# Optimization experiments

Measured on AMD Instinct MI355X. Metric: run time of the kernel, lower is better.

Reference implementation:

```python
import jax, jax.numpy as jnp
import numpy as np

S, H, NH, DS = 4096, 1024, 2, 64   # seq_len, hidden, num_heads, static_in_size
HD = H // NH                        # head_dim = 512
EPS = 1e-5                          # eqx.nn.LayerNorm default eps


def setup_inputs() -> dict:
    key = jax.random.key(0)
    ks = jax.random.split(key, 11)
    sc = lambda n: 1.0 / np.sqrt(n)
    return {
        "inputs": jax.random.normal(ks[0], (S, H), jnp.float32),
        "static_data": jax.random.normal(ks[1], (DS,), jnp.float32),
        "base_mask": jax.random.randint(ks[2], (S,), 0, 2).astype(bool),
        "Wq": jax.random.normal(ks[3], (H, H), jnp.float32) * sc(H),
        "Wk": jax.random.normal(ks[4], (H, H), jnp.float32) * sc(H),
        "Wv": jax.random.normal(ks[5], (H, H), jnp.float32) * sc(H),
        "Wo": jax.random.normal(ks[6], (H, H), jnp.float32) * sc(H),
        "Ws": jax.random.normal(ks[7], (H, DS), jnp.float32) * sc(DS),
        "bs": jax.random.normal(ks[8], (H,), jnp.float32) * 0.01,
        "ln_w": jnp.ones((H,), jnp.float32),
        "ln_b": jnp.zeros((H,), jnp.float32),
    }


def reference(inputs, static_data, base_mask, Wq, Wk, Wv, Wo, Ws, bs, ln_w, ln_b):
    # static embedding injected into keys/values
    semb = Ws @ static_data + bs                      # [H]
    kv_in = inputs + semb[None, :]                    # [S, H]

    # per-head projections (eqx Linear: y = W @ x, no bias in MHA projections)
    q = (inputs @ Wq.T).reshape(S, NH, HD)
    k = (kv_in @ Wk.T).reshape(S, NH, HD)
    v = (kv_in @ Wv.T).reshape(S, NH, HD)

    logits = jnp.einsum('qhd,khd->hqk', q, k) / np.sqrt(HD)  # [NH, S, S]

    # head 0: irregular mask (base_mask broadcast over queries); head 1: all-ones
    irregular = jnp.broadcast_to(base_mask[None, :], (S, S))
    mask = jnp.stack([irregular, jnp.ones((S, S), bool)], axis=0)  # [2, S, S]
    logits = jnp.where(mask, logits, jnp.finfo(logits.dtype).min)

    attn = jax.nn.softmax(logits, axis=-1)
    ctx = jnp.einsum('hqk,khd->qhd', attn, v).reshape(S, H)
    out = ctx @ Wo.T                                  # output projection

    # dropout_rate = 0 -> identity; residual + per-token LayerNorm
    res = out + inputs
    mu = res.mean(-1, keepdims=True)
    var = res.var(-1, keepdims=True)
    return (res - mu) / jnp.sqrt(var + EPS) * ln_w + ln_b
```

## Files before the change

kernel.cpp:

```cpp
#include <hip/hip_runtime.h>
#include <stdint.h>

#define S_LEN  4096
#define HID    1024
#define NHEAD  2
#define HDIM   512
#define NSPLIT 4
#define KS_STRIDE 520
#define LN_EPS 1e-5f

typedef __bf16 bf16x8 __attribute__((ext_vector_type(8)));
typedef float  f32x4  __attribute__((ext_vector_type(4)));

__device__ __forceinline__ float b2f(unsigned short u) {
    return __uint_as_float(((unsigned int)u) << 16);
}
__device__ __forceinline__ unsigned short f2b(float f) {
    unsigned int u = __float_as_uint(f);
    u += 0x7FFFu + ((u >> 16) & 1u);
    return (unsigned short)(u >> 16);
}

__device__ __forceinline__ void async_cp16(const void* g, void* l) {
    __builtin_amdgcn_global_load_lds(
        (const __attribute__((address_space(1))) unsigned int*)g,
        (__attribute__((address_space(3))) unsigned int*)l, 16, 0, 0);
}

__global__ void k_cvt4(const float* __restrict__ i0, const float* __restrict__ i1,
                       const float* __restrict__ i2, const float* __restrict__ i3,
                       unsigned short* __restrict__ o0, unsigned short* __restrict__ o1,
                       unsigned short* __restrict__ o2, unsigned short* __restrict__ o3) {
    int z = blockIdx.y;
    const float* in = z == 0 ? i0 : z == 1 ? i1 : z == 2 ? i2 : i3;
    unsigned short* o = z == 0 ? o0 : z == 1 ? o1 : z == 2 ? o2 : o3;
    int i = (blockIdx.x * blockDim.x + threadIdx.x) * 8;
    float4 a = *(const float4*)(in + i);
    float4 b = *(const float4*)(in + i + 4);
    unsigned short r[8] = {f2b(a.x), f2b(a.y), f2b(a.z), f2b(a.w),
                           f2b(b.x), f2b(b.y), f2b(b.z), f2b(b.w)};
    *(uint4*)(o + i) = *(const uint4*)r;
}

__global__ void k_semb(const float* __restrict__ Ws,
                       const float* __restrict__ sd,
                       const float* __restrict__ bs,
                       float* __restrict__ semb) {
    int j = blockIdx.x * blockDim.x + threadIdx.x;
    if (j >= HID) return;
    float acc = bs[j];
    const float* row = Ws + j * 64;
    #pragma unroll
    for (int d = 0; d < 64; ++d) acc += row[d] * sd[d];
    semb[j] = acc;
}

__global__ void k_kvin(const float* __restrict__ X,
                       const float* __restrict__ semb,
                       unsigned short* __restrict__ Xb,
                       unsigned short* __restrict__ kv) {
    int idx = (blockIdx.x * blockDim.x + threadIdx.x) * 8;
    if (idx >= S_LEN * HID) return;
    int col = idx & (HID - 1);
    float4 a = *(const float4*)(X + idx);
    float4 b = *(const float4*)(X + idx + 4);
    unsigned short xo[8] = {f2b(a.x), f2b(a.y), f2b(a.z), f2b(a.w),
                            f2b(b.x), f2b(b.y), f2b(b.z), f2b(b.w)};
    *(uint4*)(Xb + idx) = *(const uint4*)xo;
    unsigned short o[8];
    o[0] = f2b(a.x + semb[col + 0]);
    o[1] = f2b(a.y + semb[col + 1]);
    o[2] = f2b(a.z + semb[col + 2]);
    o[3] = f2b(a.w + semb[col + 3]);
    o[4] = f2b(b.x + semb[col + 4]);
    o[5] = f2b(b.y + semb[col + 5]);
    o[6] = f2b(b.z + semb[col + 6]);
    o[7] = f2b(b.w + semb[col + 7]);
    *(uint4*)(kv + idx) = *(const uint4*)o;
}

__device__ __forceinline__
void gemm128(const unsigned short* __restrict__ A,
             const unsigned short* __restrict__ B,
             unsigned short* __restrict__ Cb,
             int nx, int ldc) {
    __shared__ unsigned short As[128 * 32];
    __shared__ unsigned short Bs[128 * 32];
    int tid  = threadIdx.x;
    int wave = tid >> 6, lane = tid & 63;
    int quad = lane >> 4, l16 = lane & 15;
    int wm = wave >> 1, wn = wave & 1;
    int m0 = (blockIdx.x / nx) * 128, n0 = (blockIdx.x % nx) * 128;

    f32x4 zero = {0.f, 0.f, 0.f, 0.f};
    f32x4 acc[4][4];
    #pragma unroll
    for (int i = 0; i < 4; ++i)
        #pragma unroll
        for (int j = 0; j < 4; ++j) acc[i][j] = zero;

    for (int k0 = 0; k0 < HID; k0 += 32) {
        #pragma unroll
        for (int i = 0; i < 2; ++i) {
            int c = tid + i * 256;
            async_cp16(A + (m0 + (c >> 2)) * HID + k0 + (c & 3) * 8, As + c * 8);
            async_cp16(B + (n0 + (c >> 2)) * HID + k0 + (c & 3) * 8, Bs + c * 8);
        }
        __syncthreads();
        bf16x8 af[4], bfr[4];
        #pragma unroll
        for (int i = 0; i < 4; ++i)
            af[i] = *(const bf16x8*)(As + (wm * 64 + i * 16 + l16) * 32 + quad * 8);
        #pragma unroll
        for (int j = 0; j < 4; ++j)
            bfr[j] = *(const bf16x8*)(Bs + (wn * 64 + j * 16 + l16) * 32 + quad * 8);
        #pragma unroll
        for (int i = 0; i < 4; ++i)
            #pragma unroll
            for (int j = 0; j < 4; ++j)
                acc[i][j] = __builtin_amdgcn_mfma_f32_16x16x32_bf16(af[i], bfr[j], acc[i][j], 0, 0, 0);
        __syncthreads();
    }

    #pragma unroll
    for (int i = 0; i < 4; ++i) {
        int rbase = m0 + wm * 64 + i * 16 + quad * 4;
        #pragma unroll
        for (int j = 0; j < 4; ++j) {
            int col = n0 + wn * 64 + j * 16 + l16;
            #pragma unroll
            for (int r = 0; r < 4; ++r)
                Cb[(size_t)(rbase + r) * ldc + col] = f2b(acc[i][j][r]);
        }
    }
}

__global__ __launch_bounds__(256)
void k_gemm_qkv(const unsigned short* __restrict__ Xb,
                const unsigned short* __restrict__ kvin,
                const unsigned short* __restrict__ Wqb,
                const unsigned short* __restrict__ Wkb,
                const unsigned short* __restrict__ Wvb,
                unsigned short* __restrict__ Qb,
                unsigned short* __restrict__ Kb,
                unsigned short* __restrict__ Vt) {
    int z = blockIdx.z;
    if (z == 0)      gemm128(Xb,   Wqb,  Qb,  8, HID);
    else if (z == 1) gemm128(kvin, Wkb,  Kb,  8, HID);
    else             gemm128(Wvb,  kvin, Vt, 32, S_LEN);
}

__global__ __launch_bounds__(256)
void k_gemm_o(const unsigned short* __restrict__ A,
              const unsigned short* __restrict__ B,
              float* __restrict__ Cf,
              const float* __restrict__ Xres) {
    __shared__ unsigned short As[64 * 32];
    __shared__ unsigned short Bs[128 * 32];
    int tid  = threadIdx.x;
    int wave = tid >> 6, lane = tid & 63;
    int quad = lane >> 4, l16 = lane & 15;
    int m0 = (blockIdx.x >> 3) * 64, n0 = (blockIdx.x & 7) * 128;

    f32x4 zero = {0.f, 0.f, 0.f, 0.f};
    f32x4 acc[4][2];
    #pragma unroll
    for (int i = 0; i < 4; ++i)
        #pragma unroll
        for (int j = 0; j < 2; ++j) acc[i][j] = zero;

    for (int k0 = 0; k0 < HID; k0 += 32) {
        async_cp16(A + (m0 + (tid >> 2)) * HID + k0 + (tid & 3) * 8, As + tid * 8);
        #pragma unroll
        for (int i = 0; i < 2; ++i) {
            int c = tid + i * 256;
            async_cp16(B + (n0 + (c >> 2)) * HID + k0 + (c & 3) * 8, Bs + c * 8);
        }
        __syncthreads();
        bf16x8 af[4], bfr[2];
        #pragma unroll
        for (int i = 0; i < 4; ++i)
            af[i] = *(const bf16x8*)(As + (i * 16 + l16) * 32 + quad * 8);
        #pragma unroll
        for (int j = 0; j < 2; ++j)
            bfr[j] = *(const bf16x8*)(Bs + (wave * 32 + j * 16 + l16) * 32 + quad * 8);
        #pragma unroll
        for (int i = 0; i < 4; ++i)
            #pragma unroll
            for (int j = 0; j < 2; ++j)
                acc[i][j] = __builtin_amdgcn_mfma_f32_16x16x32_bf16(af[i], bfr[j], acc[i][j], 0, 0, 0);
        __syncthreads();
    }

    #pragma unroll
    for (int i = 0; i < 4; ++i) {
        int rbase = m0 + i * 16 + quad * 4;
        #pragma unroll
        for (int j = 0; j < 2; ++j) {
            int col = n0 + wave * 32 + j * 16 + l16;
            #pragma unroll
            for (int r = 0; r < 4; ++r) {
                size_t o = (size_t)(rbase + r) * HID + col;
                Cf[o] = acc[i][j][r] + Xres[o];
            }
        }
    }
}

__global__ __launch_bounds__(256, 2)
void k_flash(const unsigned short* __restrict__ Q,
             const unsigned short* __restrict__ K,
             const unsigned short* __restrict__ Vt,
             const int* __restrict__ mask,
             unsigned short* __restrict__ Opart,
             float* __restrict__ Lbuf) {
    __shared__ unsigned short Ks[2][32 * KS_STRIDE];
    __shared__ __bf16 Ps[64][40];
    int tid  = threadIdx.x;
    int wave = tid >> 6, lane = tid & 63;
    int quad = lane >> 4, l16 = lane & 15;
    int qtile = blockIdx.x, head = blockIdx.y, split = blockIdx.z;

    int qrow = qtile * 64 + wave * 16 + l16;
    const unsigned short* qp = Q + qrow * HID + head * HDIM;
    bf16x8 qf[16];
    #pragma unroll
    for (int t = 0; t < 16; ++t) qf[t] = *(const bf16x8*)(qp + t * 32 + quad * 8);

    float lsum[4];
    #pragma unroll
    for (int r = 0; r < 4; ++r) lsum[r] = 0.f;
    f32x4 zero = {0.f, 0.f, 0.f, 0.f};
    f32x4 oacc[4][8];
    #pragma unroll
    for (int mt = 0; mt < 4; ++mt)
        #pragma unroll
        for (int nt = 0; nt < 8; ++nt) oacc[mt][nt] = zero;

    const float scale = 0.044194173824159216f;
    const unsigned short* Kbase = K + head * HDIM;
    const unsigned short* Vbase = Vt + (size_t)(head * HDIM + wave * 128) * S_LEN;

    {
        int k0 = split * 1024;
        #pragma unroll
        for (int i = 0; i < 8; ++i) {
            int c = tid + i * 256;
            int row = c >> 6, col = (c & 63) * 8;
            async_cp16(Kbase + (k0 + row) * HID + col, Ks[0] + row * KS_STRIDE + col);
        }
    }

    int cur = 0;
    for (int it = 0; it < 32; ++it) {
        int k0 = split * 1024 + it * 32;
        __syncthreads();

        f32x4 sacc[2];
        sacc[0] = zero; sacc[1] = zero;
        #pragma unroll
        for (int nt = 0; nt < 2; ++nt)
            #pragma unroll
            for (int t = 0; t < 16; ++t) {
                bf16x8 kf = *(const bf16x8*)(Ks[cur] + (nt * 16 + l16) * KS_STRIDE + t * 32 + quad * 8);
                sacc[nt] = __builtin_amdgcn_mfma_f32_16x16x32_bf16(qf[t], kf, sacc[nt], 0, 0, 0);
            }

        bool keep0 = (head != 0) || (mask[k0 + l16] != 0);
        bool keep1 = (head != 0) || (mask[k0 + 16 + l16] != 0);

        #pragma unroll
        for (int r = 0; r < 4; ++r) {
            float p0 = keep0 ? __expf(fminf(sacc[0][r] * scale, 30.f)) : 0.f;
            float p1 = keep1 ? __expf(fminf(sacc[1][r] * scale, 30.f)) : 0.f;
            lsum[r] += p0 + p1;
            Ps[wave * 16 + quad * 4 + r][l16]      = (__bf16)p0;
            Ps[wave * 16 + quad * 4 + r][16 + l16] = (__bf16)p1;
        }
        __syncthreads();

        if (it < 31) {
            int kn = k0 + 32;
            #pragma unroll
            for (int i = 0; i < 8; ++i) {
                int c = tid + i * 256;
                int row = c >> 6, col = (c & 63) * 8;
                async_cp16(Kbase + (kn + row) * HID + col, Ks[cur ^ 1] + row * KS_STRIDE + col);
            }
        }

        bf16x8 pf[4];
        #pragma unroll
        for (int mt = 0; mt < 4; ++mt)
            pf[mt] = *(const bf16x8*)&Ps[mt * 16 + l16][quad * 8];
        #pragma unroll
        for (int nt = 0; nt < 8; ++nt) {
            bf16x8 vf = *(const bf16x8*)(Vbase + (size_t)(nt * 16 + l16) * S_LEN + k0 + quad * 8);
            #pragma unroll
            for (int mt = 0; mt < 4; ++mt)
                oacc[mt][nt] = __builtin_amdgcn_mfma_f32_16x16x32_bf16(pf[mt], vf, oacc[mt][nt], 0, 0, 0);
        }
        cur ^= 1;
    }

    #pragma unroll
    for (int r = 0; r < 4; ++r) {
        float s = lsum[r];
        #pragma unroll
        for (int off = 1; off < 16; off <<= 1)
            s += __shfl_xor(s, off, 64);
        lsum[r] = s;
    }
    int lrow = qtile * 64 + wave * 16 + quad * 4;
    if (l16 == 0) {
        #pragma unroll
        for (int r = 0; r < 4; ++r)
            Lbuf[(split * NHEAD + head) * S_LEN + lrow + r] = lsum[r];
    }
    unsigned short* op = Opart + (size_t)split * S_LEN * HID;
    #pragma unroll
    for (int mt = 0; mt < 4; ++mt)
        #pragma unroll
        for (int nt = 0; nt < 8; ++nt)
            #pragma unroll
            for (int r = 0; r < 4; ++r)
                op[(qtile * 64 + mt * 16 + quad * 4 + r) * HID +
                   head * HDIM + wave * 128 + nt * 16 + l16] = f2b(oacc[mt][nt][r]);
}

__global__ void k_combine(const unsigned short* __restrict__ Opart,
                          const float* __restrict__ Lbuf,
                          unsigned short* __restrict__ ctx) {
    const int SH = S_LEN * HID;
    int idx = blockIdx.x * blockDim.x + threadIdx.x;
    if (idx >= SH) return;
    int s = idx >> 10;
    int h = (idx >> 9) & 1;
    float l = 0.f, v = 0.f;
    #pragma unroll
    for (int z = 0; z < NSPLIT; ++z) {
        l += Lbuf[(z * NHEAD + h) * S_LEN + s];
        v += b2f(Opart[(size_t)z * SH + idx]);
    }
    ctx[idx] = f2b(v / l);
}

__global__ __launch_bounds__(256)
void k_ln(const float* __restrict__ res,
          const float* __restrict__ w,
          const float* __restrict__ b,
          float* __restrict__ out) {
    __shared__ float red[8];
    int s = blockIdx.x, tid = threadIdx.x;
    const float* row = res + s * HID;
    float x[4], s1 = 0.f, s2 = 0.f;
    #pragma unroll
    for (int i = 0; i < 4; ++i) {
        x[i] = row[tid + i * 256];
        s1 += x[i]; s2 += x[i] * x[i];
    }
    #pragma unroll
    for (int off = 1; off < 64; off <<= 1) {
        s1 += __shfl_xor(s1, off, 64);
        s2 += __shfl_xor(s2, off, 64);
    }
    int wave = tid >> 6;
    if ((tid & 63) == 0) { red[wave] = s1; red[4 + wave] = s2; }
    __syncthreads();
    s1 = red[0] + red[1] + red[2] + red[3];
    s2 = red[4] + red[5] + red[6] + red[7];
    float mu   = s1 * (1.f / HID);
    float var  = s2 * (1.f / HID) - mu * mu;
    float rstd = rsqrtf(var + LN_EPS);
    #pragma unroll
    for (int i = 0; i < 4; ++i) {
        int col = tid + i * 256;
        out[s * HID + col] = (x[i] - mu) * rstd * w[col] + b[col];
    }
}

extern "C" void kernel_launch(void* const* d_in, const int* in_sizes, int n_in,
                              void* d_out, int out_size, void* d_ws, size_t ws_size,
                              hipStream_t stream) {
    const float* X   = (const float*)d_in[0];
    const float* sd  = (const float*)d_in[1];
    const int*   msk = (const int*)d_in[2];
    const float* Wq  = (const float*)d_in[3];
    const float* Wk  = (const float*)d_in[4];
    const float* Wv  = (const float*)d_in[5];
    const float* Wo  = (const float*)d_in[6];
    const float* Wsp = (const float*)d_in[7];
    const float* bsp = (const float*)d_in[8];
    const float* lw  = (const float*)d_in[9];
    const float* lb  = (const float*)d_in[10];
    float* out = (float*)d_out;

    char* ws = (char*)d_ws;
    const size_t MB = 1ull << 20;
    float*          semb  = (float*)(ws);
    float*          Lbuf  = (float*)(ws + (1ull << 16));
    unsigned short* Xb    = (unsigned short*)(ws + 1 * MB);
    unsigned short* kvin  = (unsigned short*)(ws + 9 * MB);
    unsigned short* Qb    = (unsigned short*)(ws + 17 * MB);
    unsigned short* Kb    = (unsigned short*)(ws + 25 * MB);
    unsigned short* Vt    = (unsigned short*)(ws + 33 * MB);
    unsigned short* ctx   = (unsigned short*)(ws + 41 * MB);
    unsigned short* Wqb   = (unsigned short*)(ws + 49 * MB);
    unsigned short* Wkb   = (unsigned short*)(ws + 51 * MB);
    unsigned short* Wvb   = (unsigned short*)(ws + 53 * MB);
    unsigned short* Wob   = (unsigned short*)(ws + 55 * MB);
    float*          resf  = (float*)(ws + 17 * MB);
    unsigned short* Opart = (unsigned short*)(ws + 57 * MB);

    const int SH = S_LEN * HID;
    const int WW = HID * HID;

    k_cvt4<<<dim3(WW / 8 / 256, 4), dim3(256), 0, stream>>>(Wq, Wk, Wv, Wo, Wqb, Wkb, Wvb, Wob);

    k_semb<<<dim3(4), dim3(256), 0, stream>>>(Wsp, sd, bsp, semb);
    k_kvin<<<dim3(SH / 8 / 256), dim3(256), 0, stream>>>(X, semb, Xb, kvin);

    k_gemm_qkv<<<dim3(256, 1, 3), dim3(256), 0, stream>>>(Xb, kvin, Wqb, Wkb, Wvb, Qb, Kb, Vt);

    k_flash<<<dim3(S_LEN / 64, NHEAD, NSPLIT), dim3(256), 0, stream>>>(
        Qb, Kb, Vt, msk, Opart, Lbuf);
    k_combine<<<dim3(SH / 256), dim3(256), 0, stream>>>(Opart, Lbuf, ctx);

    k_gemm_o<<<dim3(512), dim3(256), 0, stream>>>(ctx, Wob, resf, X);
    k_ln<<<dim3(S_LEN), dim3(256), 0, stream>>>(resf, lw, lb, out);
}
```

Baseline: 317.0 us.

## Fuse split-K combine into output GEMM A-load and reorder flash grid

Removes the separate combine kernel: a tiny kernel computes per-row inverse softmax denominators, and the output projection GEMM sums the four bf16 partial outputs and normalizes them while staging its A tile into LDS. The flash grid is reordered so head/split vary fastest, which should improve L2 reuse of the Q tile across the blocks that share it. Half of the V fragments are now loaded before the QK MFMAs to hide their latency. The cost is that the GEMM A-load becomes synchronous, reading four times the data per tile instead of using async copies, and the early V fragments add register pressure.

```diff
diff --git a/kernel.cpp b/kernel.cpp
--- a/kernel.cpp
+++ b/kernel.cpp
@@ -150,18 +150,34 @@
     else             gemm128(Wvb,  kvin, Vt, 32, S_LEN);
 }
 
+__global__ void k_linv(const float* __restrict__ Lbuf, float* __restrict__ linv) {
+    int i = blockIdx.x * blockDim.x + threadIdx.x;
+    int h = i >> 12, s = i & (S_LEN - 1);
+    float l = 0.f;
+    #pragma unroll
+    for (int z = 0; z < NSPLIT; ++z)
+        l += Lbuf[(z * NHEAD + h) * S_LEN + s];
+    linv[i] = 1.f / l;
+}
+
 __global__ __launch_bounds__(256)
-void k_gemm_o(const unsigned short* __restrict__ A,
+void k_gemm_o(const unsigned short* __restrict__ Opart,
+              const float* __restrict__ linv,
               const unsigned short* __restrict__ B,
               float* __restrict__ Cf,
               const float* __restrict__ Xres) {
     __shared__ unsigned short As[64 * 32];
     __shared__ unsigned short Bs[128 * 32];
+    const int SH = S_LEN * HID;
     int tid  = threadIdx.x;
     int wave = tid >> 6, lane = tid & 63;
     int quad = lane >> 4, l16 = lane & 15;
     int m0 = (blockIdx.x >> 3) * 64, n0 = (blockIdx.x & 7) * 128;
 
+    int arow = tid >> 2, acol = (tid & 3) * 8;
+    float il0 = linv[m0 + arow];
+    float il1 = linv[S_LEN + m0 + arow];
+
     f32x4 zero = {0.f, 0.f, 0.f, 0.f};
     f32x4 acc[4][2];
     #pragma unroll
@@ -170,7 +186,20 @@
         for (int j = 0; j < 2; ++j) acc[i][j] = zero;
 
     for (int k0 = 0; k0 < HID; k0 += 32) {
-        async_cp16(A + (m0 + (tid >> 2)) * HID + k0 + (tid & 3) * 8, As + tid * 8);
+        int gcol = k0 + acol;
+        float il = (gcol < HDIM) ? il0 : il1;
+        float s[8] = {0.f, 0.f, 0.f, 0.f, 0.f, 0.f, 0.f, 0.f};
+        #pragma unroll
+        for (int z = 0; z < NSPLIT; ++z) {
+            uint4 t = *(const uint4*)(Opart + (size_t)z * SH + (m0 + arow) * HID + gcol);
+            const unsigned short* ts = (const unsigned short*)&t;
+            #pragma unroll
+            for (int j = 0; j < 8; ++j) s[j] += b2f(ts[j]);
+        }
+        unsigned short a8[8];
+        #pragma unroll
+        for (int j = 0; j < 8; ++j) a8[j] = f2b(s[j] * il);
+        *(uint4*)(As + tid * 8) = *(const uint4*)a8;
         #pragma unroll
         for (int i = 0; i < 2; ++i) {
             int c = tid + i * 256;
@@ -219,7 +248,7 @@
     int tid  = threadIdx.x;
     int wave = tid >> 6, lane = tid & 63;
     int quad = lane >> 4, l16 = lane & 15;
-    int qtile = blockIdx.x, head = blockIdx.y, split = blockIdx.z;
+    int head = blockIdx.x / NSPLIT, split = blockIdx.x % NSPLIT, qtile = blockIdx.y;
 
     int qrow = qtile * 64 + wave * 16 + l16;
     const unsigned short* qp = Q + qrow * HID + head * HDIM;
@@ -255,6 +284,11 @@
     for (int it = 0; it < 32; ++it) {
         int k0 = split * 1024 + it * 32;
         __syncthreads();
+
+        bf16x8 vfe[4];
+        #pragma unroll
+        for (int nt = 0; nt < 4; ++nt)
+            vfe[nt] = *(const bf16x8*)(Vbase + (size_t)(nt * 16 + l16) * S_LEN + k0 + quad * 8);
 
         f32x4 sacc[2];
         sacc[0] = zero; sacc[1] = zero;
@@ -295,7 +329,8 @@
             pf[mt] = *(const bf16x8*)&Ps[mt * 16 + l16][quad * 8];
         #pragma unroll
         for (int nt = 0; nt < 8; ++nt) {
-            bf16x8 vf = *(const bf16x8*)(Vbase + (size_t)(nt * 16 + l16) * S_LEN + k0 + quad * 8);
+            bf16x8 vf = (nt < 4) ? vfe[nt]
+                : *(const bf16x8*)(Vbase + (size_t)(nt * 16 + l16) * S_LEN + k0 + quad * 8);
             #pragma unroll
             for (int mt = 0; mt < 4; ++mt)
                 oacc[mt][nt] = __builtin_amdgcn_mfma_f32_16x16x32_bf16(pf[mt], vf, oacc[mt][nt], 0, 0, 0);
@@ -326,23 +361,6 @@
             for (int r = 0; r < 4; ++r)
                 op[(qtile * 64 + mt * 16 + quad * 4 + r) * HID +
                    head * HDIM + wave * 128 + nt * 16 + l16] = f2b(oacc[mt][nt][r]);
-}
-
-__global__ void k_combine(const unsigned short* __restrict__ Opart,
-                          const float* __restrict__ Lbuf,
-                          unsigned short* __restrict__ ctx) {
-    const int SH = S_LEN * HID;
-    int idx = blockIdx.x * blockDim.x + threadIdx.x;
-    if (idx >= SH) return;
-    int s = idx >> 10;
-    int h = (idx >> 9) & 1;
-    float l = 0.f, v = 0.f;
-    #pragma unroll
-    for (int z = 0; z < NSPLIT; ++z) {
-        l += Lbuf[(z * NHEAD + h) * S_LEN + s];
-        v += b2f(Opart[(size_t)z * SH + idx]);
-    }
-    ctx[idx] = f2b(v / l);
 }
 
 __global__ __launch_bounds__(256)
@@ -399,12 +417,12 @@
     const size_t MB = 1ull << 20;
     float*          semb  = (float*)(ws);
     float*          Lbuf  = (float*)(ws + (1ull << 16));
+    float*          linv  = (float*)(ws + (8ull << 16));
     unsigned short* Xb    = (unsigned short*)(ws + 1 * MB);
     unsigned short* kvin  = (unsigned short*)(ws + 9 * MB);
     unsigned short* Qb    = (unsigned short*)(ws + 17 * MB);
     unsigned short* Kb    = (unsigned short*)(ws + 25 * MB);
     unsigned short* Vt    = (unsigned short*)(ws + 33 * MB);
-    unsigned short* ctx   = (unsigned short*)(ws + 41 * MB);
     unsigned short* Wqb   = (unsigned short*)(ws + 49 * MB);
     unsigned short* Wkb   = (unsigned short*)(ws + 51 * MB);
     unsigned short* Wvb   = (unsigned short*)(ws + 53 * MB);
@@ -422,10 +440,10 @@
 
     k_gemm_qkv<<<dim3(256, 1, 3), dim3(256), 0, stream>>>(Xb, kvin, Wqb, Wkb, Wvb, Qb, Kb, Vt);
 
-    k_flash<<<dim3(S_LEN / 64, NHEAD, NSPLIT), dim3(256), 0, stream>>>(
+    k_flash<<<dim3(NHEAD * NSPLIT, S_LEN / 64), dim3(256), 0, stream>>>(
         Qb, Kb, Vt, msk, Opart, Lbuf);
-    k_combine<<<dim3(SH / 256), dim3(256), 0, stream>>>(Opart, Lbuf, ctx);
-
-    k_gemm_o<<<dim3(512), dim3(256), 0, stream>>>(ctx, Wob, resf, X);
+
+    k_linv<<<dim3(NHEAD * S_LEN / 256), dim3(256), 0, stream>>>(Lbuf, linv);
+    k_gemm_o<<<dim3(512), dim3(256), 0, stream>>>(Opart, linv, Wob, resf, X);
     k_ln<<<dim3(S_LEN), dim3(256), 0, stream>>>(resf, lw, lb, out);
 }
```

Result: no change. 323.1 us (+1.9%).
